# Performance work log

Hardware: AMD Instinct MI355X
Metric: run time of the kernel (lower is better)

## Reference

```python
import jax, jax.numpy as jnp
import numpy as np

R = 7        # rcnn_crop_size[cls_ind]
SCALE = 4    # cfg['stride']


def _pool1d(x, c0, c1, K):
    # Adaptive max pool along leading axis of x ([F, ...] -> [R, ...]).
    # torch AdaptiveMaxPool bins: start_i = floor(i*L/R), end_i = ceil((i+1)*L/R)
    F = x.shape[0]
    L = c1 - c0
    i = jnp.arange(R)
    starts = c0 + (i * L) // R
    ends = c0 + ((i + 1) * L + R - 1) // R
    idx = starts[:, None] + jnp.arange(K)[None, :]           # [R, K], K bounds max bin length
    g = x[jnp.clip(idx, 0, F - 1)]                           # [R, K, ...]
    valid = (idx < ends[:, None]).reshape((R, K) + (1,) * (x.ndim - 1))
    return jnp.max(jnp.where(valid, g, jnp.finfo(x.dtype).min), axis=1)


def _crop_pool(f, dims_max, p, Ks):
    # One proposal: variable-size crop from f[b] + adaptive max pool to [C,R,R,R].
    b = p[0].astype(jnp.int32)
    center, side = p[2:5], p[5:8]
    c0 = jnp.floor((center - side / 2) / SCALE).astype(jnp.int32)
    c1 = jnp.ceil((center + side / 2) / SCALE).astype(jnp.int32)
    c0 = jnp.maximum(c0, 0)
    c1 = jnp.minimum(c1, dims_max)
    x = f[b]                                                 # [C, Fd, Fh, Fw]
    for ax in range(3):                                      # separable adaptive max pool
        x = jnp.moveaxis(x, ax + 1, 0)
        x = _pool1d(x, c0[ax], c1[ax], Ks[ax])
        x = jnp.moveaxis(x, 0, ax + 1)
    return x                                                 # [C, R, R, R]


def setup_inputs() -> dict:
    key = jax.random.key(0)
    kf, kb, ks, kc, kd = jax.random.split(key, 5)
    B, C, Fs = 4, 64, 32
    N = 96
    f = jax.random.normal(kf, (B, C, Fs, Fs, Fs), dtype=jnp.float32)
    inputs = jnp.zeros((B, 1, 128, 128, 128), dtype=jnp.float32)
    bidx = jax.random.randint(kb, (N, 1), 0, B).astype(jnp.float32)
    score = jax.random.uniform(ks, (N, 1), dtype=jnp.float32)
    centers = jax.random.uniform(kc, (N, 3), minval=24.0, maxval=104.0, dtype=jnp.float32)
    sides = jax.random.uniform(kd, (N, 3), minval=8.0, maxval=48.0, dtype=jnp.float32)
    proposals = jnp.concatenate([bidx, score, centers, sides], axis=1)  # [N, 8]
    return {"f": f, "inputs": inputs, "proposals": proposals, "cls_ind": 0}


def reference(f, inputs, proposals, cls_ind):
    D, H, W = inputs.shape[2], inputs.shape[3], inputs.shape[4]
    dims_max = jnp.array([D // SCALE, H // SCALE, W // SCALE], dtype=jnp.int32)
    # max bin length per axis for any crop length L <= F: ceil(F/R)+1
    Ks = tuple(-(-f.shape[ax + 2] // R) + 1 for ax in range(3))
    return jax.vmap(lambda p: _crop_pool(f, dims_max, p, Ks))(proposals)  # [N, C, R, R, R]
```

## Files before the change

### kernel.cpp

```cpp
#include <hip/hip_runtime.h>
#include <float.h>


#define NTHREADS 256
#define NCH 4
#define MAXL 14
#define MAXV (MAXL * MAXL * MAXL)
#define BATCH 8

__global__ __launch_bounds__(NTHREADS) void crop_roi_v4(
        const float* __restrict__ f,
        const float* __restrict__ props,
        float* __restrict__ out,
        int C) {
    __shared__ float s[NCH * MAXV];
    const int cbase = blockIdx.x * NCH;
    const int n = blockIdx.y;
    const int tid = threadIdx.x;

    const float* p = props + (size_t)n * 8;
    const int b = (int)p[0];

    int d0 = (int)floorf((p[2] - p[5] * 0.5f) * 0.25f);
    int d1 = (int)ceilf ((p[2] + p[5] * 0.5f) * 0.25f);
    int h0 = (int)floorf((p[3] - p[6] * 0.5f) * 0.25f);
    int h1 = (int)ceilf ((p[3] + p[6] * 0.5f) * 0.25f);
    int w0 = (int)floorf((p[4] - p[7] * 0.5f) * 0.25f);
    int w1 = (int)ceilf ((p[4] + p[7] * 0.5f) * 0.25f);
    d0 = max(d0, 0); d1 = min(d1, 32);
    h0 = max(h0, 0); h1 = min(h1, 32);
    w0 = max(w0, 0); w1 = min(w1, 32);
    const int Ld = d1 - d0, Lh = h1 - h0, Lw = w1 - w0;

    const float* base0 = f + (((size_t)b * C + cbase) << 15);
    const int nch = min(NCH, C - cbase);

    size_t choff[NCH];
#pragma unroll
    for (int cs = 0; cs < NCH; ++cs)
        choff[cs] = (size_t)min(cs, nch - 1) << 15;

    if (Ld <= MAXL && Lh <= MAXL && Lw <= MAXL) {
        const int D1 = Lh * Lw;
        const int V  = Ld * D1;
        const unsigned Mdh = (D1 > 1) ? (unsigned)(0x100000000ULL / (unsigned)D1) + 1u : 0u;
        const unsigned Mw  = (Lw > 1) ? (unsigned)(0x100000000ULL / (unsigned)Lw) + 1u : 0u;

        for (int e0 = tid; e0 < V; e0 += NTHREADS * BATCH) {
            int ec[BATCH], g[BATCH];
#pragma unroll
            for (int u = 0; u < BATCH; ++u) {
                int e = e0 + u * NTHREADS;
                e = min(e, V - 1);
                ec[u] = e;
                unsigned d = (D1 > 1) ? __umulhi((unsigned)e, Mdh) : (unsigned)e;
                unsigned r = (unsigned)e - d * (unsigned)D1;
                unsigned h = (Lw > 1) ? __umulhi(r, Mw) : r;
                unsigned w = r - h * (unsigned)Lw;
                g[u] = ((((d0 + (int)d) << 5) + (h0 + (int)h)) << 5) + (w0 + (int)w);
            }
            float rv[BATCH][NCH];
#pragma unroll
            for (int u = 0; u < BATCH; ++u)
#pragma unroll
                for (int cs = 0; cs < NCH; ++cs)
                    rv[u][cs] = base0[choff[cs] + g[u]];
#pragma unroll
            for (int u = 0; u < BATCH; ++u)
#pragma unroll
                for (int cs = 0; cs < NCH; ++cs)
                    s[cs * MAXV + ec[u]] = rv[u][cs];
        }
        __syncthreads();

        for (int o = tid; o < 343; o += NTHREADS) {
            const int i = o / 49;
            const int j = (o / 7) % 7;
            const int k = o % 7;
            const int a0 = (i * Ld) / 7,  a1 = ((i + 1) * Ld + 6) / 7;
            const int b0 = (j * Lh) / 7,  b1 = ((j + 1) * Lh + 6) / 7;
            const int g0 = (k * Lw) / 7,  g1 = ((k + 1) * Lw + 6) / 7;
            float m[NCH];
#pragma unroll
            for (int cs = 0; cs < NCH; ++cs) m[cs] = -FLT_MAX;
            for (int d = a0; d < a1; ++d) {
                for (int h = b0; h < b1; ++h) {
                    const int rowb = (d * Lh + h) * Lw;
                    for (int w = g0; w < g1; ++w) {
                        const int idx = rowb + w;
#pragma unroll
                        for (int cs = 0; cs < NCH; ++cs)
                            m[cs] = fmaxf(m[cs], s[cs * MAXV + idx]);
                    }
                }
            }
            for (int cs = 0; cs < nch; ++cs)
                out[((size_t)n * C + cbase + cs) * 343 + o] = m[cs];
        }
    } else {
        for (int o = tid; o < 343; o += NTHREADS) {
            const int i = o / 49, j = (o / 7) % 7, k = o % 7;
            const int ds = d0 + (i * Ld) / 7, de = d0 + ((i + 1) * Ld + 6) / 7;
            const int hs = h0 + (j * Lh) / 7, he = h0 + ((j + 1) * Lh + 6) / 7;
            const int ws = w0 + (k * Lw) / 7, we = w0 + ((k + 1) * Lw + 6) / 7;
            for (int cs = 0; cs < nch; ++cs) {
                float m = -FLT_MAX;
                const float* basec = base0 + ((size_t)cs << 15);
                for (int d = ds; d < de; ++d)
                    for (int h = hs; h < he; ++h) {
                        const float* row = basec + (d << 10) + (h << 5);
                        for (int w = ws; w < we; ++w) m = fmaxf(m, row[w]);
                    }
                out[((size_t)n * C + cbase + cs) * 343 + o] = m;
            }
        }
    }
}

extern "C" void kernel_launch(void* const* d_in, const int* in_sizes, int n_in,
                              void* d_out, int out_size, void* d_ws, size_t ws_size,
                              hipStream_t stream) {
    const float* f = (const float*)d_in[0];
    const float* props = (const float*)d_in[2];

    int N = in_sizes[2] / 8;
    int C = out_size / (N * 343);

    dim3 block(NTHREADS);
    dim3 grid((C + NCH - 1) / NCH, N);
    crop_roi_v4<<<grid, block, 0, stream>>>(f, props, (float*)d_out, C);
}
```

Measured before the change: 106.3 us.

## Shrink shared crop buffer, single-pass gather, unroll fixed 3x3x3 bin max

Cuts the shared-memory crop bound from 14 to 13 per axis. This lowers per-block LDS use and may allow more resident blocks per CU. The batch size is raised so one pass of 256x9 loads covers the whole crop with no outer loop, and `__launch_bounds__(256, 4)` is added to request higher occupancy. The pooling loops become a fully unrolled 3x3x3 sample with clamped, duplicated indices, which is valid because bins are at most 3 long when L is 13 or less. Larger crops still take the slower global-memory fallback, and the extra register pressure from the unrolled batch could cause spills.

```diff
diff --git a/kernel.cpp b/kernel.cpp
--- a/kernel.cpp
+++ b/kernel.cpp
@@ -4,11 +4,11 @@
 
 #define NTHREADS 256
 #define NCH 4
-#define MAXL 14
+#define MAXL 13
 #define MAXV (MAXL * MAXL * MAXL)
-#define BATCH 8
+#define BATCH 9
 
-__global__ __launch_bounds__(NTHREADS) void crop_roi_v4(
+__global__ __launch_bounds__(NTHREADS, 4) void crop_roi_v7(
         const float* __restrict__ f,
         const float* __restrict__ props,
         float* __restrict__ out,
@@ -40,36 +40,37 @@
     for (int cs = 0; cs < NCH; ++cs)
         choff[cs] = (size_t)min(cs, nch - 1) << 15;
 
-    if (Ld <= MAXL && Lh <= MAXL && Lw <= MAXL) {
+    if (Ld >= 1 && Ld <= MAXL && Lh >= 1 && Lh <= MAXL && Lw >= 1 && Lw <= MAXL) {
         const int D1 = Lh * Lw;
         const int V  = Ld * D1;
         const unsigned Mdh = (D1 > 1) ? (unsigned)(0x100000000ULL / (unsigned)D1) + 1u : 0u;
         const unsigned Mw  = (Lw > 1) ? (unsigned)(0x100000000ULL / (unsigned)Lw) + 1u : 0u;
 
-        for (int e0 = tid; e0 < V; e0 += NTHREADS * BATCH) {
-            int ec[BATCH], g[BATCH];
+        float rv[BATCH][NCH];
+        int   ec[BATCH];
 #pragma unroll
-            for (int u = 0; u < BATCH; ++u) {
-                int e = e0 + u * NTHREADS;
-                e = min(e, V - 1);
-                ec[u] = e;
+        for (int u = 0; u < BATCH; ++u) {
+            const int e = tid + u * NTHREADS;
+            if (e < V) {
                 unsigned d = (D1 > 1) ? __umulhi((unsigned)e, Mdh) : (unsigned)e;
                 unsigned r = (unsigned)e - d * (unsigned)D1;
                 unsigned h = (Lw > 1) ? __umulhi(r, Mw) : r;
                 unsigned w = r - h * (unsigned)Lw;
-                g[u] = ((((d0 + (int)d) << 5) + (h0 + (int)h)) << 5) + (w0 + (int)w);
-            }
-            float rv[BATCH][NCH];
-#pragma unroll
-            for (int u = 0; u < BATCH; ++u)
+                const int g = ((((d0 + (int)d) << 5) + (h0 + (int)h)) << 5)
+                              + w0 + (int)w;
+                ec[u] = e;
 #pragma unroll
                 for (int cs = 0; cs < NCH; ++cs)
-                    rv[u][cs] = base0[choff[cs] + g[u]];
+                    rv[u][cs] = base0[choff[cs] + g];
+            }
+        }
 #pragma unroll
-            for (int u = 0; u < BATCH; ++u)
+        for (int u = 0; u < BATCH; ++u) {
+            if (tid + u * NTHREADS < V) {
 #pragma unroll
                 for (int cs = 0; cs < NCH; ++cs)
                     s[cs * MAXV + ec[u]] = rv[u][cs];
+            }
         }
         __syncthreads();
 
@@ -80,14 +81,20 @@
             const int a0 = (i * Ld) / 7,  a1 = ((i + 1) * Ld + 6) / 7;
             const int b0 = (j * Lh) / 7,  b1 = ((j + 1) * Lh + 6) / 7;
             const int g0 = (k * Lw) / 7,  g1 = ((k + 1) * Lw + 6) / 7;
+            const int dd[3] = { a0, min(a0 + 1, a1 - 1), a1 - 1 };
+            const int hh[3] = { b0, min(b0 + 1, b1 - 1), b1 - 1 };
+            const int ww[3] = { g0, min(g0 + 1, g1 - 1), g1 - 1 };
             float m[NCH];
 #pragma unroll
             for (int cs = 0; cs < NCH; ++cs) m[cs] = -FLT_MAX;
-            for (int d = a0; d < a1; ++d) {
-                for (int h = b0; h < b1; ++h) {
-                    const int rowb = (d * Lh + h) * Lw;
-                    for (int w = g0; w < g1; ++w) {
-                        const int idx = rowb + w;
+#pragma unroll
+            for (int x = 0; x < 3; ++x) {
+#pragma unroll
+                for (int y = 0; y < 3; ++y) {
+                    const int rowb = (dd[x] * Lh + hh[y]) * Lw;
+#pragma unroll
+                    for (int z = 0; z < 3; ++z) {
+                        const int idx = rowb + ww[z];
 #pragma unroll
                         for (int cs = 0; cs < NCH; ++cs)
                             m[cs] = fmaxf(m[cs], s[cs * MAXV + idx]);
@@ -128,5 +135,5 @@
 
     dim3 block(NTHREADS);
     dim3 grid((C + NCH - 1) / NCH, N);
-    crop_roi_v4<<<grid, block, 0, stream>>>(f, props, (float*)d_out, C);
+    crop_roi_v7<<<grid, block, 0, stream>>>(f, props, (float*)d_out, C);
 }
```

Measured after the change: 102.8 us. -3.3%, faster.
